# Optimization experiments

Measured on AMD Instinct MI355X. Metric: run time of the kernel, lower is better.

The kernel has to match this reference:

```python
import jax, jax.numpy as jnp
import numpy as np

LN_EPS = 1e-5


def layer_norm(x, gamma, beta):
    mu = jnp.mean(x, axis=-1, keepdims=True)
    var = jnp.var(x, axis=-1, keepdims=True)
    return (x - mu) * jax.lax.rsqrt(var + LN_EPS) * gamma + beta


def setup_inputs() -> dict:
    key = jax.random.key(0)
    ks = jax.random.split(key, 8)
    d = 768
    B, H, W = 8, 32, 32
    s = 1.0 / np.sqrt(d)
    inp = {
        "x": jax.random.normal(ks[0], (B, d, H, W), dtype=jnp.float32),
        "Wq": jax.random.normal(ks[1], (d, d), dtype=jnp.float32) * s,
        "bq": jnp.zeros((d,), jnp.float32),
        "Wk": jax.random.normal(ks[2], (d, d), dtype=jnp.float32) * s,
        "bk": jnp.zeros((d,), jnp.float32),
        "Wv": jax.random.normal(ks[3], (d, d), dtype=jnp.float32) * s,
        "bv": jnp.zeros((d,), jnp.float32),
        "Wo": jax.random.normal(ks[4], (d, d), dtype=jnp.float32) * s,
        "bo": jnp.zeros((d,), jnp.float32),
        "Wg": jax.random.normal(ks[5], (d, d), dtype=jnp.float32) * s,
        "bg": jnp.zeros((d,), jnp.float32),
        "gamma": jnp.ones((d,), jnp.float32),
        "beta": jnp.zeros((d,), jnp.float32),
    }
    return inp


def reference(x, Wq, bq, Wk, bk, Wv, bv, Wo, bo, Wg, bg, gamma, beta):
    n_heads = 12
    B, C, H, W = x.shape
    T = H * W
    d_head = C // n_heads
    # (B, C, H, W) -> (B, T, C)
    xt = x.reshape(B, C, T).transpose(0, 2, 1)
    xn = layer_norm(xt, gamma, beta)
    # torch Linear: x @ W.T + b
    q = xn @ Wq.T + bq
    k = xn @ Wk.T + bk
    v = xn @ Wv.T + bv

    def split_heads(t):
        return t.reshape(B, T, n_heads, d_head).transpose(0, 2, 1, 3)  # (B, nH, T, dh)

    q, k, v = split_heads(q), split_heads(k), split_heads(v)
    scale = 1.0 / np.sqrt(d_head).astype(np.float32)
    scores = jnp.einsum("bhtd,bhsd->bhts", q, k) * scale  # (B, nH, T, T)
    probs = jax.nn.softmax(scores, axis=-1)
    y = jnp.einsum("bhts,bhsd->bhtd", probs, v)  # (B, nH, T, dh)
    # headwise + elementwise gate over full d_model
    gate = jax.nn.sigmoid(xn @ Wg.T + bg)  # (B, T, C)
    gate = gate.reshape(B, T, n_heads, d_head).transpose(0, 2, 1, 3)
    y = y * gate
    y = y.transpose(0, 2, 1, 3).reshape(B, T, C)
    out = y @ Wo.T + bo  # (B, T, C)
    return out.transpose(0, 2, 1).reshape(B, C, H, W)
```

## Files before the change

### kernel.cpp

```cpp
#include <hip/hip_runtime.h>
#include <math.h>

#define B_   8
#define C_   768
#define T_   1024
#define BT_  (B_*T_)
#define WSZ  (C_*C_)

using f16x8 = __attribute__((ext_vector_type(8))) _Float16;
using f32x4 = __attribute__((ext_vector_type(4))) float;
typedef unsigned short u16;

__device__ inline u16 f16b(float x) {
    _Float16 h = (_Float16)x;
    return __builtin_bit_cast(u16, h);
}
__device__ inline float f16f(u16 b) {
    return (float)__builtin_bit_cast(_Float16, b);
}

__global__ __launch_bounds__(256) void wconv_all(
    const float* __restrict__ W0, const float* __restrict__ W1,
    const float* __restrict__ W2, const float* __restrict__ W3,
    const float* __restrict__ W4, u16* __restrict__ wbuf) {
    int mat = blockIdx.y;
    const float* W = (mat == 0) ? W0 : (mat == 1) ? W1 : (mat == 2) ? W2
                   : (mat == 3) ? W3 : W4;
    u16* o = wbuf + (size_t)mat * WSZ;
    int i = (blockIdx.x * 256 + threadIdx.x) * 4;
    float4 w = *(const float4*)(W + i);
    ushort4 h;
    h.x = f16b(w.x);
    h.y = f16b(w.y);
    h.z = f16b(w.z);
    h.w = f16b(w.w);
    *(ushort4*)(o + i) = h;
}

__global__ __launch_bounds__(256) void ln_kernel(const float* __restrict__ x,
                                                 const float* __restrict__ gamma,
                                                 const float* __restrict__ beta,
                                                 u16* __restrict__ xh) {
    int b = blockIdx.y;
    int t0 = blockIdx.x * 16;
    int tid = threadIdx.x;
    int tx = tid & 15;
    int cg = tid >> 4;
    const float* xb = x + (size_t)b * C_ * T_ + t0 + tx;

    float v[48];
    float s = 0.f, sq = 0.f;
    #pragma unroll
    for (int i = 0; i < 48; ++i) {
        float val = xb[(size_t)(i * 16 + cg) * T_];
        v[i] = val; s += val; sq += val * val;
    }
    __shared__ float rs_[16][16], rq_[16][16];
    rs_[cg][tx] = s;
    rq_[cg][tx] = sq;
    __syncthreads();
    __shared__ float mu_[16], rstd_[16];
    if (tid < 16) {
        float S = 0.f, Q = 0.f;
        #pragma unroll
        for (int k = 0; k < 16; ++k) { S += rs_[k][tid]; Q += rq_[k][tid]; }
        float mu = S * (1.0f / 768.0f);
        float var = Q * (1.0f / 768.0f) - mu * mu;
        mu_[tid] = mu;
        rstd_[tid] = 1.0f / sqrtf(var + 1e-5f);
    }
    __syncthreads();
    float mu = mu_[tx], rstd = rstd_[tx];
    __shared__ u16 Lt[16][776];
    #pragma unroll
    for (int i = 0; i < 48; ++i) {
        int c = i * 16 + cg;
        Lt[tx][c] = f16b((v[i] - mu) * rstd * gamma[c] + beta[c]);
    }
    __syncthreads();
    size_t obase = ((size_t)b * 1024 + t0) * C_;
    #pragma unroll
    for (int st = 0; st < 12; ++st) {
        int idx = st * 256 + tid;
        int t = idx / 192, c4 = idx % 192;
        *(ushort4*)(xh + obase + (size_t)t * C_ + c4 * 4) = *(ushort4*)&Lt[t][c4 * 4];
    }
}

__global__ __launch_bounds__(256, 3) void qkvg_mfma(
    const u16* __restrict__ xh, const u16* __restrict__ wmats,
    const float* __restrict__ bq, const float* __restrict__ bk,
    const float* __restrict__ bv, const float* __restrict__ bg,
    u16* __restrict__ qh, u16* __restrict__ kh,
    u16* __restrict__ vth, u16* __restrict__ g) {
    int bx = blockIdx.x;
    int by = blockIdx.y;
    int mat = by / 6;
    int n0  = (by % 6) * 128;
    int m0  = bx * 128;
    const u16* Wh = wmats + (size_t)mat * WSZ;
    const float* bias = (mat == 0) ? bq : (mat == 1) ? bk : (mat == 2) ? bv : bg;

    __shared__ __attribute__((aligned(16))) u16 Ah[2 * 4096], Bh[2 * 4096];

    int tid  = threadIdx.x;
    int lane = tid & 63, wid = tid >> 6;
    int wm = (wid & 1) * 64, wn = (wid >> 1) * 64;
    int fr = lane & 15, rq = (lane >> 4) * 4;

    f32x4 acc[4][4];
    #pragma unroll
    for (int i = 0; i < 4; ++i)
        #pragma unroll
        for (int j = 0; j < 4; ++j)
            acc[i][j] = (f32x4){0.f, 0.f, 0.f, 0.f};

    int j = tid >> 5, u = tid & 31;
    size_t offA = (size_t)(m0 + j * 16 + (u & 15)) * 768 + (u >> 4) * 8;
    size_t offB = (size_t)(n0 + j * 16 + (u & 15)) * 768 + (u >> 4) * 8;
    int lo0 = j * 512 + u * 8;
    int ba = (wm >> 4), bb2 = (wn >> 4);

    uint4 a0, a1, c0, c1;
    #define LOADT(T) do { int kk0 = (T) * 32; \
        a0 = *(const uint4*)(xh + offA + kk0); \
        a1 = *(const uint4*)(xh + offA + kk0 + 16); \
        c0 = *(const uint4*)(Wh + offB + kk0); \
        c1 = *(const uint4*)(Wh + offB + kk0 + 16); \
    } while (0)
    #define STORET(BUF) do { int lb = (BUF) * 4096 + lo0; \
        *(uint4*)(Ah + lb) = a0;  *(uint4*)(Ah + lb + 256) = a1; \
        *(uint4*)(Bh + lb) = c0;  *(uint4*)(Bh + lb + 256) = c1; \
    } while (0)

    LOADT(0);
    STORET(0);
    LOADT(1);
    __syncthreads();
    int cur = 0;
    for (int t = 0; t < 24; ++t) {
        int nxt = cur ^ 1;
        STORET(nxt);
        LOADT((t + 2 < 24) ? t + 2 : 0);
        int cb = cur * 4096;
        f16x8 fah[4], fbh[4];
        #pragma unroll
        for (int i = 0; i < 4; ++i) {
            fah[i] = *(const f16x8*)(Ah + cb + (ba + i) * 512 + lane * 8);
            fbh[i] = *(const f16x8*)(Bh + cb + (bb2 + i) * 512 + lane * 8);
        }
        if (mat == 2) {
            #pragma unroll
            for (int mi = 0; mi < 4; ++mi)
                #pragma unroll
                for (int ni = 0; ni < 4; ++ni)
                    acc[mi][ni] = __builtin_amdgcn_mfma_f32_16x16x32_f16(fbh[ni], fah[mi], acc[mi][ni], 0, 0, 0);
        } else {
            #pragma unroll
            for (int mi = 0; mi < 4; ++mi)
                #pragma unroll
                for (int ni = 0; ni < 4; ++ni)
                    acc[mi][ni] = __builtin_amdgcn_mfma_f32_16x16x32_f16(fah[mi], fbh[ni], acc[mi][ni], 0, 0, 0);
        }
        __syncthreads();
        cur = nxt;
    }
    #undef LOADT
    #undef STORET
    if (mat == 2) {
        int bb = m0 >> 10;
        #pragma unroll
        for (int mi = 0; mi < 4; ++mi) {
            int tok = m0 + wm + mi * 16 + fr;
            int tl  = tok & 1023;
            #pragma unroll
            for (int ni = 0; ni < 4; ++ni) {
                #pragma unroll
                for (int rg = 0; rg < 4; ++rg) {
                    int ch = n0 + wn + ni * 16 + rq + rg;
                    float val = acc[mi][ni][rg] + bias[ch];
                    size_t addr = ((size_t)((bb * 12 + (ch >> 6)) * 64 + (ch & 63))) * 1024 + tl;
                    vth[addr] = f16b(val);
                }
            }
        }
    } else {
        u16* oh = (mat == 0) ? qh : (mat == 1) ? kh : g;
        float scale = (mat == 0) ? 0.125f : 1.0f;
        #pragma unroll
        for (int ni = 0; ni < 4; ++ni) {
            int col = n0 + wn + ni * 16 + fr;
            float bb = bias[col];
            #pragma unroll
            for (int mi = 0; mi < 4; ++mi) {
                int row = m0 + wm + mi * 16 + rq;
                #pragma unroll
                for (int rg = 0; rg < 4; ++rg) {
                    float val = (acc[mi][ni][rg] + bb) * scale;
                    oh[(size_t)(row + rg) * 768 + col] = f16b(val);
                }
            }
        }
    }
}

__global__ __launch_bounds__(256, 2) void attn_mfma(
    const u16* __restrict__ qhg, const u16* __restrict__ khg,
    const u16* __restrict__ vthg, const u16* __restrict__ gbf,
    u16* __restrict__ yh) {
    int qt = blockIdx.x;
    int h  = blockIdx.y;
    int b  = blockIdx.z;
    __shared__ u16 Kh[2 * 4096], Vh[2 * 4096];
    __shared__ u16 Ps[64 * 72];
    int tid = threadIdx.x;
    int lane = tid & 63, w = tid >> 6;
    int fr = lane & 15, quad = lane >> 4, fq = quad * 8;

    size_t qbaseA = ((size_t)(b * 1024 + qt * 128)) * 768 + h * 64;
    size_t qbaseB = qbaseA + (size_t)64 * 768;
    size_t kbase = ((size_t)(b * 1024)) * 768 + h * 64;
    size_t vbase = ((size_t)((b * 12 + h) * 64)) * 1024;

    f16x8 aqA[2], aqB[2];
    #pragma unroll
    for (int kk = 0; kk < 2; ++kk) {
        size_t ro = (size_t)(w * 16 + fr) * 768 + kk * 32 + fq;
        aqA[kk] = *(const f16x8*)(qhg + qbaseA + ro);
        aqB[kk] = *(const f16x8*)(qhg + qbaseB + ro);
    }

    float m_A = -1e30f, l_A = 0.0f, m_B = -1e30f, l_B = 0.0f;
    f32x4 OA[4], OB[4];
    #pragma unroll
    for (int i = 0; i < 4; ++i) {
        OA[i] = (f32x4){0.f, 0.f, 0.f, 0.f};
        OB[i] = (f32x4){0.f, 0.f, 0.f, 0.f};
    }

    int j = tid >> 5, u = tid & 31;
    int kk_ = j >> 2, nd_ = j & 3;
    size_t offK = kbase + (size_t)(nd_ * 16 + (u & 15)) * 768 + kk_ * 32 + (u >> 4) * 8;
    size_t offV = vbase + (size_t)(nd_ * 16 + (u & 15)) * 1024 + kk_ * 32 + (u >> 4) * 8;
    int lo0 = j * 512 + u * 8;

    uint4 rk0, rk1, rv0, rv1;
    #define LOADKV(ST) do { \
        size_t ok = offK + (size_t)(ST) * 49152; \
        size_t ov = offV + (size_t)(ST) * 64; \
        rk0 = *(const uint4*)(khg + ok);  rk1 = *(const uint4*)(khg + ok + 16); \
        rv0 = *(const uint4*)(vthg + ov); rv1 = *(const uint4*)(vthg + ov + 16); \
    } while (0)
    #define STOREKV(BUF) do { \
        int lb = (BUF) * 4096 + lo0; \
        *(uint4*)(Kh + lb) = rk0;  *(uint4*)(Kh + lb + 256) = rk1; \
        *(uint4*)(Vh + lb) = rv0;  *(uint4*)(Vh + lb + 256) = rv1; \
    } while (0)

    #define STRIP(AQ, MS, LS, OACC) do { \
        f32x4 sacc[4]; \
        _Pragma("unroll") \
        for (int nt = 0; nt < 4; ++nt) sacc[nt] = (f32x4){0.f, 0.f, 0.f, 0.f}; \
        _Pragma("unroll") \
        for (int nt = 0; nt < 4; ++nt) \
            _Pragma("unroll") \
            for (int kk = 0; kk < 2; ++kk) { \
                f16x8 kb = *(const f16x8*)(Kh + cur * 4096 + (kk * 4 + nt) * 512 + lane * 8); \
                sacc[nt] = __builtin_amdgcn_mfma_f32_16x16x32_f16(kb, AQ[kk], sacc[nt], 0, 0, 0); \
            } \
        float mx = -1e30f; \
        _Pragma("unroll") \
        for (int nt = 0; nt < 4; ++nt) \
            _Pragma("unroll") \
            for (int rg = 0; rg < 4; ++rg) mx = fmaxf(mx, sacc[nt][rg]); \
        mx = fmaxf(mx, __shfl_xor(mx, 16)); \
        mx = fmaxf(mx, __shfl_xor(mx, 32)); \
        float mn = fmaxf(MS, mx); \
        float al = __expf(MS - mn); \
        MS = mn; \
        float rs = 0.0f; \
        _Pragma("unroll") \
        for (int nt = 0; nt < 4; ++nt) \
            _Pragma("unroll") \
            for (int rg = 0; rg < 4; ++rg) { \
                float p = __expf(sacc[nt][rg] - mn); \
                sacc[nt][rg] = p; \
                rs += p; \
            } \
        rs += __shfl_xor(rs, 16); \
        rs += __shfl_xor(rs, 32); \
        LS = LS * al + rs; \
        int prow = (w * 16 + fr) * 72; \
        _Pragma("unroll") \
        for (int nt = 0; nt < 4; ++nt) { \
            ushort4 hp; \
            hp.x = f16b(sacc[nt][0]); \
            hp.y = f16b(sacc[nt][1]); \
            hp.z = f16b(sacc[nt][2]); \
            hp.w = f16b(sacc[nt][3]); \
            *(ushort4*)&Ps[prow + nt * 16 + quad * 4] = hp; \
        } \
        float alr[4]; \
        _Pragma("unroll") \
        for (int rg = 0; rg < 4; ++rg) alr[rg] = __shfl(al, quad * 4 + rg, 16); \
        _Pragma("unroll") \
        for (int dn = 0; dn < 4; ++dn) \
            _Pragma("unroll") \
            for (int rg = 0; rg < 4; ++rg) OACC[dn][rg] *= alr[rg]; \
        _Pragma("unroll") \
        for (int kk = 0; kk < 2; ++kk) { \
            f16x8 pa = *(const f16x8*)&Ps[(w * 16 + fr) * 72 + fq + kk * 32]; \
            _Pragma("unroll") \
            for (int dn = 0; dn < 4; ++dn) { \
                f16x8 vb = *(const f16x8*)(Vh + cur * 4096 + (kk * 4 + dn) * 512 + lane * 8); \
                OACC[dn] = __builtin_amdgcn_mfma_f32_16x16x32_f16(pa, vb, OACC[dn], 0, 0, 0); \
            } \
        } \
    } while (0)

    LOADKV(0);
    STOREKV(0);
    LOADKV(1);
    __syncthreads();
    int cur = 0;
    for (int st = 0; st < 16; ++st) {
        int nxt = cur ^ 1;
        STOREKV(nxt);
        int s2 = (st + 2 < 16) ? (st + 2) : 0;
        LOADKV(s2);
        STRIP(aqA, m_A, l_A, OA);
        STRIP(aqB, m_B, l_B, OB);
        __syncthreads();
        cur = nxt;
    }
    #undef LOADKV
    #undef STOREKV
    #undef STRIP
    float invA[4], invB[4];
    #pragma unroll
    for (int rg = 0; rg < 4; ++rg) {
        invA[rg] = 1.0f / __shfl(l_A, quad * 4 + rg, 16);
        invB[rg] = 1.0f / __shfl(l_B, quad * 4 + rg, 16);
    }
    int tokA0 = b * 1024 + qt * 128 + w * 16;
    #pragma unroll
    for (int dn = 0; dn < 4; ++dn) {
        int ch = h * 64 + dn * 16 + fr;
        #pragma unroll
        for (int rg = 0; rg < 4; ++rg) {
            int tok = tokA0 + quad * 4 + rg;
            float gv = f16f(gbf[(size_t)tok * 768 + ch]);
            float sg = 1.0f / (1.0f + __expf(-gv));
            yh[(size_t)tok * 768 + ch] = f16b(OA[dn][rg] * invA[rg] * sg);
            int tok2 = tok + 64;
            float gv2 = f16f(gbf[(size_t)tok2 * 768 + ch]);
            float sg2 = 1.0f / (1.0f + __expf(-gv2));
            yh[(size_t)tok2 * 768 + ch] = f16b(OB[dn][rg] * invB[rg] * sg2);
        }
    }
}

__global__ __launch_bounds__(256, 3) void out_mfma(
    const u16* __restrict__ yh, const u16* __restrict__ woh,
    const float* __restrict__ bo, float* __restrict__ out) {
    int bx = blockIdx.x;
    int by = blockIdx.y;
    int m0 = bx * 128;
    int n0 = by * 128;

    __shared__ __attribute__((aligned(16))) u16 Ah[2 * 4096], Bh[2 * 4096];

    int tid  = threadIdx.x;
    int lane = tid & 63, wid = tid >> 6;
    int wm = (wid & 1) * 64, wn = (wid >> 1) * 64;
    int fr = lane & 15, rq = (lane >> 4) * 4;

    f32x4 acc[4][4];
    #pragma unroll
    for (int i = 0; i < 4; ++i)
        #pragma unroll
        for (int j = 0; j < 4; ++j)
            acc[i][j] = (f32x4){0.f, 0.f, 0.f, 0.f};

    int j = tid >> 5, u = tid & 31;
    size_t offA = (size_t)(m0 + j * 16 + (u & 15)) * 768 + (u >> 4) * 8;
    size_t offB = (size_t)(n0 + j * 16 + (u & 15)) * 768 + (u >> 4) * 8;
    int lo0 = j * 512 + u * 8;
    int ba = (wm >> 4), bb2 = (wn >> 4);

    uint4 a0, a1, c0, c1;
    #define LOADT(T) do { int kk0 = (T) * 32; \
        a0 = *(const uint4*)(woh + offA + kk0); \
        a1 = *(const uint4*)(woh + offA + kk0 + 16); \
        c0 = *(const uint4*)(yh + offB + kk0); \
        c1 = *(const uint4*)(yh + offB + kk0 + 16); \
    } while (0)
    #define STORET(BUF) do { int lb = (BUF) * 4096 + lo0; \
        *(uint4*)(Ah + lb) = a0;  *(uint4*)(Ah + lb + 256) = a1; \
        *(uint4*)(Bh + lb) = c0;  *(uint4*)(Bh + lb + 256) = c1; \
    } while (0)

    LOADT(0);
    STORET(0);
    LOADT(1);
    __syncthreads();
    int cur = 0;
    for (int t = 0; t < 24; ++t) {
        int nxt = cur ^ 1;
        STORET(nxt);
        LOADT((t + 2 < 24) ? t + 2 : 0);
        int cb = cur * 4096;
        f16x8 fah[4], fbh[4];
        #pragma unroll
        for (int i = 0; i < 4; ++i) {
            fah[i] = *(const f16x8*)(Ah + cb + (ba + i) * 512 + lane * 8);
            fbh[i] = *(const f16x8*)(Bh + cb + (bb2 + i) * 512 + lane * 8);
        }
        #pragma unroll
        for (int mi = 0; mi < 4; ++mi)
            #pragma unroll
            for (int ni = 0; ni < 4; ++ni)
                acc[mi][ni] = __builtin_amdgcn_mfma_f32_16x16x32_f16(fah[mi], fbh[ni], acc[mi][ni], 0, 0, 0);
        __syncthreads();
        cur = nxt;
    }
    #undef LOADT
    #undef STORET
    int bb = n0 >> 10;
    #pragma unroll
    for (int ni = 0; ni < 4; ++ni) {
        int colg = n0 + wn + ni * 16 + fr;
        int tl = colg & 1023;
        #pragma unroll
        for (int mi = 0; mi < 4; ++mi) {
            int row = m0 + wm + mi * 16 + rq;
            #pragma unroll
            for (int rg = 0; rg < 4; ++rg) {
                float val = acc[mi][ni][rg] + bo[row + rg];
                out[((size_t)bb * 768 + row + rg) * 1024 + tl] = val;
            }
        }
    }
}

extern "C" void kernel_launch(void* const* d_in, const int* in_sizes, int n_in,
                              void* d_out, int out_size, void* d_ws, size_t ws_size,
                              hipStream_t stream) {
    const float* x     = (const float*)d_in[0];
    const float* Wq    = (const float*)d_in[1];
    const float* bq    = (const float*)d_in[2];
    const float* Wk    = (const float*)d_in[3];
    const float* bk    = (const float*)d_in[4];
    const float* Wv    = (const float*)d_in[5];
    const float* bv    = (const float*)d_in[6];
    const float* Wo    = (const float*)d_in[7];
    const float* bo    = (const float*)d_in[8];
    const float* Wg    = (const float*)d_in[9];
    const float* bg    = (const float*)d_in[10];
    const float* gamma = (const float*)d_in[11];
    const float* beta  = (const float*)d_in[12];
    float* out = (float*)d_out;

    const size_t S = (size_t)BT_ * C_;
    u16* xn   = (u16*)d_ws;
    u16* qh   = xn + S;
    u16* kh   = qh + S;
    u16* vth  = kh + S;
    u16* g_bf = vth + S;
    u16* wbuf = g_bf + S;
    u16* y_h  = xn;

    wconv_all<<<dim3(WSZ / 1024, 5), 256, 0, stream>>>(Wq, Wk, Wv, Wg, Wo, wbuf);
    ln_kernel<<<dim3(64, 8), 256, 0, stream>>>(x, gamma, beta, xn);
    qkvg_mfma<<<dim3(64, 24), 256, 0, stream>>>(xn, wbuf, bq, bk, bv, bg,
                                                qh, kh, vth, g_bf);
    attn_mfma<<<dim3(8, 12, 8), 256, 0, stream>>>(qh, kh, vth, g_bf, y_h);
    out_mfma<<<dim3(6, 64), 256, 0, stream>>>(y_h, wbuf + (size_t)4 * WSZ, bo, out);
}
```

Before: 298.9 us.

## Stage attention K/V tiles via direct global-to-LDS loads and raise occupancy

```diff
diff --git a/kernel.cpp b/kernel.cpp
--- a/kernel.cpp
+++ b/kernel.cpp
@@ -17,6 +17,12 @@
 }
 __device__ inline float f16f(u16 b) {
     return (float)__builtin_bit_cast(_Float16, b);
+}
+
+typedef const __attribute__((address_space(1))) unsigned int gas_uint;
+typedef __attribute__((address_space(3))) unsigned int las_uint;
+__device__ inline void gld16(const u16* __restrict__ g, u16* l) {
+    __builtin_amdgcn_global_load_lds((gas_uint*)g, (las_uint*)l, 16, 0, 0);
 }
 
 __global__ __launch_bounds__(256) void wconv_all(
@@ -204,14 +210,14 @@
     }
 }
 
-__global__ __launch_bounds__(256, 2) void attn_mfma(
+__global__ __launch_bounds__(256, 3) void attn_mfma(
     const u16* __restrict__ qhg, const u16* __restrict__ khg,
     const u16* __restrict__ vthg, const u16* __restrict__ gbf,
     u16* __restrict__ yh) {
     int qt = blockIdx.x;
     int h  = blockIdx.y;
     int b  = blockIdx.z;
-    __shared__ u16 Kh[2 * 4096], Vh[2 * 4096];
+    __shared__ __attribute__((aligned(16))) u16 Kh[2 * 4096], Vh[2 * 4096];
     __shared__ u16 Ps[64 * 72];
     int tid = threadIdx.x;
     int lane = tid & 63, w = tid >> 6;
@@ -238,23 +244,23 @@
         OB[i] = (f32x4){0.f, 0.f, 0.f, 0.f};
     }
 
-    int j = tid >> 5, u = tid & 31;
-    int kk_ = j >> 2, nd_ = j & 3;
-    size_t offK = kbase + (size_t)(nd_ * 16 + (u & 15)) * 768 + kk_ * 32 + (u >> 4) * 8;
-    size_t offV = vbase + (size_t)(nd_ * 16 + (u & 15)) * 1024 + kk_ * 32 + (u >> 4) * 8;
-    int lo0 = j * 512 + u * 8;
-
-    uint4 rk0, rk1, rv0, rv1;
-    #define LOADKV(ST) do { \
-        size_t ok = offK + (size_t)(ST) * 49152; \
-        size_t ov = offV + (size_t)(ST) * 64; \
-        rk0 = *(const uint4*)(khg + ok);  rk1 = *(const uint4*)(khg + ok + 16); \
-        rv0 = *(const uint4*)(vthg + ov); rv1 = *(const uint4*)(vthg + ov + 16); \
-    } while (0)
-    #define STOREKV(BUF) do { \
-        int lb = (BUF) * 4096 + lo0; \
-        *(uint4*)(Kh + lb) = rk0;  *(uint4*)(Kh + lb + 256) = rk1; \
-        *(uint4*)(Vh + lb) = rv0;  *(uint4*)(Vh + lb + 256) = rv1; \
+    int f0 = 2 * w;
+    int f1 = f0 + 1;
+    const u16* kgA = khg + kbase + (size_t)((f0 & 3) * 16 + fr) * 768 + (f0 >> 2) * 32 + (lane >> 4) * 8;
+    const u16* kgB = khg + kbase + (size_t)((f1 & 3) * 16 + fr) * 768 + (f1 >> 2) * 32 + (lane >> 4) * 8;
+    const u16* vgA = vthg + vbase + (size_t)((f0 & 3) * 16 + fr) * 1024 + (f0 >> 2) * 32 + (lane >> 4) * 8;
+    const u16* vgB = vthg + vbase + (size_t)((f1 & 3) * 16 + fr) * 1024 + (f1 >> 2) * 32 + (lane >> 4) * 8;
+    int ldA = f0 * 512 + lane * 8;
+    int ldB = ldA + 512;
+
+    #define STAGE(ST, BUF) do { \
+        size_t ko = (size_t)(ST) * 49152; \
+        size_t vo = (size_t)(ST) * 64; \
+        int bo_ = (BUF) * 4096; \
+        gld16(kgA + ko, Kh + bo_ + ldA); \
+        gld16(kgB + ko, Kh + bo_ + ldB); \
+        gld16(vgA + vo, Vh + bo_ + ldA); \
+        gld16(vgB + vo, Vh + bo_ + ldB); \
     } while (0)
 
     #define STRIP(AQ, MS, LS, OACC) do { \
@@ -318,23 +324,18 @@
         } \
     } while (0)
 
-    LOADKV(0);
-    STOREKV(0);
-    LOADKV(1);
+    STAGE(0, 0);
     __syncthreads();
     int cur = 0;
     for (int st = 0; st < 16; ++st) {
         int nxt = cur ^ 1;
-        STOREKV(nxt);
-        int s2 = (st + 2 < 16) ? (st + 2) : 0;
-        LOADKV(s2);
+        if (st + 1 < 16) STAGE(st + 1, nxt);
         STRIP(aqA, m_A, l_A, OA);
         STRIP(aqB, m_B, l_B, OB);
         __syncthreads();
         cur = nxt;
     }
-    #undef LOADKV
-    #undef STOREKV
+    #undef STAGE
     #undef STRIP
     float invA[4], invB[4];
     #pragma unroll
```

New measurement: 299.5 us. No clear change (+0.2%).
